# Kernel optimization log

Measured on AMD Instinct MI355X. Metric: run time of the kernel, lower is better.

Reference implementation:

```python
import jax, jax.numpy as jnp
import numpy as np

V, EMB, ENC, DEC = 50000, 256, 512, 512
E2 = ENC * 2            # bidirectional encoder output dim = 1024
B, S1, S2 = 128, 200, 200
NEG = -1e10


def _bahdanau(hidden, enc_out, mask, W, b, v):
    # hidden [B,DEC], enc_out [S,B,E2], mask [B,S] -> weights [B,S]
    S = enc_out.shape[0]
    h = jnp.broadcast_to(hidden[None], (S,) + hidden.shape)          # [S,B,DEC]
    energy = jnp.tanh(jnp.concatenate([h, enc_out], axis=-1) @ W + b)  # [S,B,DEC]
    scores = energy @ v                                              # [S,B]
    scores = jnp.where(mask.T == 0, NEG, scores)
    return jax.nn.softmax(scores, axis=0).T                          # [B,S]


def setup_inputs() -> dict:
    key = jax.random.key(0)
    ks = jax.random.split(key, 20)
    f = lambda k, shp, s=0.05: jax.random.normal(k, shp, dtype=jnp.float32) * s
    inp = {
        "input": jax.random.randint(ks[0], (B,), 0, V),
        "hidden": f(ks[1], (B, DEC), 1.0),
        "src1": jax.random.randint(ks[2], (S1, B), 0, V),
        "encoder_outputs1": f(ks[3], (S1, B, E2), 1.0),
        "mask1": jnp.ones((B, S1), dtype=jnp.int32),
        "triple_mask": jnp.ones((B, S1), dtype=jnp.int32),
        "encoder_outputs2": f(ks[4], (S2, B, E2), 1.0),
        "mask2": jnp.ones((B, S2), dtype=jnp.int32),
        # parameters
        "embedding": f(ks[5], (V, EMB)),
        "attn_W": f(ks[6], (E2 + DEC, DEC)),
        "attn_b": jnp.zeros((DEC,), jnp.float32),
        "attn_v": f(ks[7], (DEC,)),
        "copy_W": f(ks[8], (E2 + DEC, DEC)),
        "copy_b": jnp.zeros((DEC,), jnp.float32),
        "copy_v": f(ks[9], (DEC,)),
        "gru_Wih": f(ks[10], (3 * DEC, E2 + EMB)),
        "gru_Whh": f(ks[11], (3 * DEC, DEC)),
        "gru_bih": jnp.zeros((3 * DEC,), jnp.float32),
        "gru_bhh": jnp.zeros((3 * DEC,), jnp.float32),
        "fc_W": f(ks[12], (V, E2 + DEC)),
        "fc_b": jnp.zeros((V,), jnp.float32),
        "gate_W": f(ks[13], (1, E2 + EMB)),
        "gate_b": jnp.zeros((1,), jnp.float32),
    }
    return inp


def reference(input, hidden, src1, encoder_outputs1, mask1, triple_mask,
              encoder_outputs2, mask2, embedding, attn_W, attn_b, attn_v,
              copy_W, copy_b, copy_v, gru_Wih, gru_Whh, gru_bih, gru_bhh,
              fc_W, fc_b, gate_W, gate_b):
    # embed current token (dropout = identity at eval)
    emb = embedding[input]                                           # [B,EMB]
    # joint attention over concatenated encoders
    enc = jnp.concatenate([encoder_outputs1, encoder_outputs2], axis=0)  # [S1+S2,B,E2]
    mask = jnp.concatenate([mask1, mask2], axis=1)                   # [B,S1+S2]
    a = _bahdanau(hidden, enc, mask, attn_W, attn_b, attn_v)         # [B,S1+S2]
    weighted = jnp.einsum('bs,sbe->be', a, enc)                      # [B,E2]
    # single-step GRU (PyTorch gate layout: r, z, n)
    x = jnp.concatenate([emb, weighted], axis=-1)                    # [B,E2+EMB]
    gx = x @ gru_Wih.T + gru_bih
    gh = hidden @ gru_Whh.T + gru_bhh
    xr, xz, xn = jnp.split(gx, 3, axis=-1)
    hr, hz, hn = jnp.split(gh, 3, axis=-1)
    r = jax.nn.sigmoid(xr + hr)
    z = jax.nn.sigmoid(xz + hz)
    n = jnp.tanh(xn + r * hn)
    h_new = (1.0 - z) * n + z * hidden                               # [B,DEC]
    # generation distribution
    state = jnp.concatenate([h_new, weighted], axis=1)               # [B,DEC+E2]
    vocab_dist = jax.nn.softmax(state @ fc_W.T + fc_b, axis=-1)      # [B,V]
    # copy gate + copy attention over encoder 1 only
    p_gen = jax.nn.sigmoid(jnp.concatenate([weighted, emb], axis=-1) @ gate_W.T + gate_b)  # [B,1]
    attn_dist = _bahdanau(h_new, encoder_outputs1, mask1 * triple_mask,
                          copy_W, copy_b, copy_v)                    # [B,S1]
    vd = p_gen * vocab_dist
    ad = (1.0 - p_gen) * attn_dist
    # scatter_add copy probabilities into vocab slots
    b_idx = jnp.arange(vd.shape[0])[:, None]                         # [B,1]
    final_dist = vd.at[b_idx, src1.T].add(ad)                        # [B,V]
    return final_dist, h_new
```

## Files before the change

kernel.cpp:

```cpp
#include <hip/hip_runtime.h>
#include <math.h>

#define BB   128
#define DECD 512
#define E2D  1024
#define EMBD 256
#define S1D  200
#define S2D  200
#define SJD  400
#define VV   50000
#define NEGV (-1e10f)
#define JY   800

typedef unsigned short u16;
typedef __bf16 bf16x8 __attribute__((ext_vector_type(8)));
typedef float f32x4 __attribute__((ext_vector_type(4)));
typedef u16 u16x8 __attribute__((ext_vector_type(8)));

__device__ __forceinline__ u16 f2bf(float x) {
  unsigned u = __float_as_uint(x);
  unsigned r = (u + 0x7fffu + ((u >> 16) & 1u)) >> 16;
  return (u16)r;
}
__device__ __forceinline__ float bf2f(u16 h) {
  return __uint_as_float(((unsigned)h) << 16);
}

typedef const __attribute__((address_space(1))) void* gas_t;
typedef __attribute__((address_space(3))) void* las_t;
__device__ __forceinline__ void async_copy16(const u16* g, u16* l) {
  __builtin_amdgcn_global_load_lds((gas_t)g, (las_t)l, 16, 0, 0);
}

__global__ __launch_bounds__(256) void k_cvt(const float* __restrict__ src,
    u16* __restrict__ dst, int n8) {
  int i = blockIdx.x * 256 + threadIdx.x;
  if (i >= n8) return;
  const float4 f0 = *(const float4*)(src + (size_t)i * 8);
  const float4 f1 = *(const float4*)(src + (size_t)i * 8 + 4);
  u16x8 o;
  o[0] = f2bf(f0.x); o[1] = f2bf(f0.y); o[2] = f2bf(f0.z); o[3] = f2bf(f0.w);
  o[4] = f2bf(f1.x); o[5] = f2bf(f1.y); o[6] = f2bf(f1.z); o[7] = f2bf(f1.w);
  *(u16x8*)(dst + (size_t)i * 8) = o;
}

__global__ __launch_bounds__(256) void k_wt2(const float* __restrict__ Wa,
    const float* __restrict__ Wc, u16* __restrict__ Wta, u16* __restrict__ Wtc) {
  __shared__ float t[32][33];
  const float* W = blockIdx.z ? Wc : Wa;
  u16* Wt = blockIdx.z ? Wtc : Wta;
  int bk = blockIdx.x, bn = blockIdx.y;
  int tx = threadIdx.x & 31, ty = threadIdx.x >> 5;
  #pragma unroll
  for (int r = 0; r < 4; ++r) {
    int k = bk * 32 + ty + r * 8;
    t[ty + r * 8][tx] = W[(size_t)(512 + k) * 512 + bn * 32 + tx];
  }
  __syncthreads();
  #pragma unroll
  for (int r = 0; r < 4; ++r) {
    int n = bn * 32 + ty + r * 8;
    Wt[(size_t)n * 1024 + bk * 32 + tx] = f2bf(t[tx][ty + r * 8]);
  }
}

__global__ __launch_bounds__(256) void gemm_energy_jc(
    const float* __restrict__ enc1, const float* __restrict__ enc2,
    const u16* __restrict__ BtA, const u16* __restrict__ BtC,
    const float* __restrict__ hW, const float* __restrict__ v,
    float* __restrict__ partJ, float* __restrict__ preC) {
  __shared__ u16 As[2][64 * 32];
  __shared__ u16 Bs[256 * 32];
  __shared__ float sbuf[64][2];
  int tid = threadIdx.x;
  int wid = tid >> 6, lane = tid & 63;
  int wr = wid >> 1, wc = wid & 1;
  int bn = blockIdx.x;
  int jy = blockIdx.y;
  int joint = (jy < JY);
  size_t m0 = joint ? (size_t)jy * 64 : (size_t)(jy - JY) * 64;
  int bhalf = (jy & 1) * 64;
  int n0 = bn * 256;

  int rA = tid >> 2, cslot = tid & 3;
  int lAoff = rA * 32 + ((cslot ^ ((rA >> 1) & 3)) * 8);
  const float* base;
  if (joint)
    base = (m0 < (size_t)S1D * BB) ? (enc1 + m0 * E2D)
                                   : (enc2 + (m0 - (size_t)S1D * BB) * E2D);
  else
    base = enc1 + m0 * E2D;
  const float* gA_f = base + (size_t)rA * E2D + cslot * 8;

  const u16* Bt = joint ? BtA : BtC;
  const u16* gB[4];
  #pragma unroll
  for (int i = 0; i < 4; ++i) {
    int rn = i * 64 + wid * 16 + (lane >> 2);
    int c = (lane & 3) ^ ((rn >> 1) & 3);
    gB[i] = Bt + (size_t)(n0 + rn) * E2D + c * 8;
  }

  int q = lane >> 4, cl = lane & 15;
  int aoff[2], boff[8];
  #pragma unroll
  for (int mi = 0; mi < 2; ++mi) {
    int row = wr * 32 + mi * 16 + cl;
    aoff[mi] = row * 64 + ((q ^ ((row >> 1) & 3)) * 16);
  }
  #pragma unroll
  for (int nj = 0; nj < 8; ++nj) {
    int rn = wc * 128 + nj * 16 + cl;
    boff[nj] = rn * 64 + ((q ^ ((rn >> 1) & 3)) * 16);
  }

  f32x4 acc[2][8];
  #pragma unroll
  for (int mi = 0; mi < 2; ++mi)
    #pragma unroll
    for (int nj = 0; nj < 8; ++nj) {
      f32x4 z = {0.f, 0.f, 0.f, 0.f};
      acc[mi][nj] = z;
    }

  float4 a0 = *(const float4*)(gA_f);
  float4 a1 = *(const float4*)(gA_f + 4);
  {
    u16x8 ob;
    ob[0] = f2bf(a0.x); ob[1] = f2bf(a0.y); ob[2] = f2bf(a0.z); ob[3] = f2bf(a0.w);
    ob[4] = f2bf(a1.x); ob[5] = f2bf(a1.y); ob[6] = f2bf(a1.z); ob[7] = f2bf(a1.w);
    *(u16x8*)(&As[0][lAoff]) = ob;
  }
  a0 = *(const float4*)(gA_f + 32);
  a1 = *(const float4*)(gA_f + 36);

  for (int t = 0; t < 32; ++t) {
    int cur = t & 1, nxt = cur ^ 1;
    int k0 = t * 32, k1 = k0 + 32;
    #pragma unroll
    for (int i = 0; i < 4; ++i) async_copy16(gB[i] + k0, &Bs[2048 * i + wid * 512]);
    if (t < 31) {
      u16x8 ob;
      ob[0] = f2bf(a0.x); ob[1] = f2bf(a0.y); ob[2] = f2bf(a0.z); ob[3] = f2bf(a0.w);
      ob[4] = f2bf(a1.x); ob[5] = f2bf(a1.y); ob[6] = f2bf(a1.z); ob[7] = f2bf(a1.w);
      *(u16x8*)(&As[nxt][lAoff]) = ob;
      if (t < 30) {
        a0 = *(const float4*)(gA_f + k1 + 32);
        a1 = *(const float4*)(gA_f + k1 + 36);
      }
    }
    __syncthreads();
    bf16x8 af[2];
    #pragma unroll
    for (int mi = 0; mi < 2; ++mi)
      af[mi] = *(const bf16x8*)((const char*)As[cur] + aoff[mi]);
    #pragma unroll
    for (int nj = 0; nj < 8; ++nj) {
      bf16x8 bg = *(const bf16x8*)((const char*)Bs + boff[nj]);
      acc[0][nj] = __builtin_amdgcn_mfma_f32_16x16x32_bf16(af[0], bg, acc[0][nj], 0, 0, 0);
      acc[1][nj] = __builtin_amdgcn_mfma_f32_16x16x32_bf16(af[1], bg, acc[1][nj], 0, 0, 0);
    }
    __syncthreads();
  }

  if (joint) {
    #pragma unroll
    for (int mi = 0; mi < 2; ++mi) {
      #pragma unroll
      for (int j = 0; j < 4; ++j) {
        int m = wr * 32 + mi * 16 + q * 4 + j;
        float s = 0.f;
        #pragma unroll
        for (int nj = 0; nj < 8; ++nj) {
          int d = n0 + wc * 128 + nj * 16 + cl;
          s += tanhf(acc[mi][nj][j] + hW[(size_t)(bhalf + m) * DECD + d]) * v[d];
        }
        s += __shfl_xor(s, 1, 64);
        s += __shfl_xor(s, 2, 64);
        s += __shfl_xor(s, 4, 64);
        s += __shfl_xor(s, 8, 64);
        if (cl == 0) sbuf[m][wc] = s;
      }
    }
    __syncthreads();
    if (tid < 64)
      partJ[(size_t)bn * 51200 + m0 + tid] = sbuf[tid][0] + sbuf[tid][1];
  } else {
    #pragma unroll
    for (int mi = 0; mi < 2; ++mi) {
      #pragma unroll
      for (int nj = 0; nj < 8; ++nj) {
        int d = n0 + wc * 128 + nj * 16 + cl;
        #pragma unroll
        for (int j = 0; j < 4; ++j) {
          int m = wr * 32 + mi * 16 + q * 4 + j;
          preC[(m0 + m) * (size_t)DECD + d] = acc[mi][nj][j];
        }
      }
    }
  }
}

__global__ __launch_bounds__(256) void k_copy_epi(const float* __restrict__ preC,
    const float* __restrict__ hWc, const float* __restrict__ v,
    float* __restrict__ scC) {
  int r = blockIdx.x * 4 + (threadIdx.x >> 6);
  int lane = threadIdx.x & 63;
  int b = r & 127, s = r >> 7;
  const float* pr = preC + (size_t)r * DECD + lane * 8;
  const float* hr = hWc + (size_t)b * DECD + lane * 8;
  const float* vr = v + lane * 8;
  float4 p0 = *(const float4*)(pr),     p1 = *(const float4*)(pr + 4);
  float4 h0 = *(const float4*)(hr),     h1 = *(const float4*)(hr + 4);
  float4 v0 = *(const float4*)(vr),     v1 = *(const float4*)(vr + 4);
  float acc = tanhf(p0.x + h0.x) * v0.x + tanhf(p0.y + h0.y) * v0.y
            + tanhf(p0.z + h0.z) * v0.z + tanhf(p0.w + h0.w) * v0.w
            + tanhf(p1.x + h1.x) * v1.x + tanhf(p1.y + h1.y) * v1.y
            + tanhf(p1.z + h1.z) * v1.z + tanhf(p1.w + h1.w) * v1.w;
  #pragma unroll
  for (int off = 32; off > 0; off >>= 1) acc += __shfl_xor(acc, off, 64);
  if (lane == 0) scC[(size_t)b * S1D + s] = acc;
}

__global__ __launch_bounds__(256) void k_softmax_j(const float* __restrict__ part,
    int M, float* __restrict__ sc,
    const int* __restrict__ m1, const int* __restrict__ m2) {
  int b = blockIdx.x, tid = threadIdx.x;
  __shared__ float sm[4];
  int s0 = tid, s2 = tid + 256;
  float a0 = -INFINITY, a1 = -INFINITY;
  {
    int msk = (s0 < S1D) ? m1[b * S1D + s0] : m2[b * S2D + (s0 - S1D)];
    int m = s0 * 128 + b;
    a0 = msk ? (part[m] + part[M + m]) : NEGV;
  }
  if (s2 < SJD) {
    int msk = (s2 < S1D) ? m1[b * S1D + s2] : m2[b * S2D + (s2 - S1D)];
    int m = s2 * 128 + b;
    a1 = msk ? (part[m] + part[M + m]) : NEGV;
  }
  float vmax = fmaxf(a0, a1);
  #pragma unroll
  for (int off = 32; off > 0; off >>= 1) vmax = fmaxf(vmax, __shfl_down(vmax, off, 64));
  int lane = tid & 63, wid = tid >> 6;
  if (lane == 0) sm[wid] = vmax;
  __syncthreads();
  vmax = fmaxf(fmaxf(sm[0], sm[1]), fmaxf(sm[2], sm[3]));
  __syncthreads();
  float lsum = expf(a0 - vmax);
  if (s2 < SJD) lsum += expf(a1 - vmax);
  #pragma unroll
  for (int off = 32; off > 0; off >>= 1) lsum += __shfl_down(lsum, off, 64);
  if (lane == 0) sm[wid] = lsum;
  __syncthreads();
  float inv = 1.0f / (sm[0] + sm[1] + sm[2] + sm[3]);
  sc[(size_t)b * SJD + s0] = expf(a0 - vmax) * inv;
  if (s2 < SJD) sc[(size_t)b * SJD + s2] = expf(a1 - vmax) * inv;
}

__global__ __launch_bounds__(256) void k_softmax_s(float* __restrict__ sc, int S,
    const int* __restrict__ m1, const int* __restrict__ m2) {
  int b = blockIdx.x, tid = threadIdx.x;
  __shared__ float sm[4];
  int s0 = tid;
  float a0 = -INFINITY;
  if (s0 < S) {
    int msk = m1[b * S + s0] * m2[b * S + s0];
    a0 = msk ? sc[(size_t)b * S + s0] : NEGV;
  }
  float vmax = a0;
  #pragma unroll
  for (int off = 32; off > 0; off >>= 1) vmax = fmaxf(vmax, __shfl_down(vmax, off, 64));
  int lane = tid & 63, wid = tid >> 6;
  if (lane == 0) sm[wid] = vmax;
  __syncthreads();
  vmax = fmaxf(fmaxf(sm[0], sm[1]), fmaxf(sm[2], sm[3]));
  __syncthreads();
  float lsum = (s0 < S) ? expf(a0 - vmax) : 0.f;
  #pragma unroll
  for (int off = 32; off > 0; off >>= 1) lsum += __shfl_down(lsum, off, 64);
  if (lane == 0) sm[wid] = lsum;
  __syncthreads();
  float inv = 1.0f / (sm[0] + sm[1] + sm[2] + sm[3]);
  if (s0 < S) sc[(size_t)b * S + s0] = expf(a0 - vmax) * inv;
}

__device__ __forceinline__ void fc2_body(
    const u16* __restrict__ A, const float* __restrict__ Bf,
    const float* __restrict__ bias, float* __restrict__ C,
    int N, int K, int n0) {
  __shared__ u16 As[2][128 * 32];
  __shared__ u16 Bs[2][128 * 32];
  int tid = threadIdx.x;
  int wid = tid >> 6, lane = tid & 63;
  int wr = wid >> 2, wc = wid & 3;

  int rowa = wid * 16 + (lane >> 2);
  int ca = (lane & 3) ^ ((rowa >> 1) & 3);
  const u16* gA = A + (size_t)rowa * K + ca * 8;

  int rB = tid >> 2, cB = tid & 3;
  int gnB = n0 + rB; if (gnB >= N) gnB = N - 1;
  const float* gB = Bf + (size_t)gnB * K + cB * 8;
  int lBoff = rB * 32 + ((cB ^ ((rB >> 1) & 3)) * 8);

  int q = lane >> 4, cl = lane & 15;
  int aoff[4], boff[2];
  #pragma unroll
  for (int mi = 0; mi < 4; ++mi) {
    int row = wr * 64 + mi * 16 + cl;
    aoff[mi] = row * 64 + ((q ^ ((row >> 1) & 3)) * 16);
  }
  #pragma unroll
  for (int nj = 0; nj < 2; ++nj) {
    int rn = wc * 32 + nj * 16 + cl;
    boff[nj] = rn * 64 + ((q ^ ((rn >> 1) & 3)) * 16);
  }

  f32x4 acc[4][2];
  #pragma unroll
  for (int mi = 0; mi < 4; ++mi)
    #pragma unroll
    for (int nj = 0; nj < 2; ++nj) {
      f32x4 z = {0.f, 0.f, 0.f, 0.f};
      acc[mi][nj] = z;
    }

  for (int k0 = 0; k0 < K; k0 += 64) {
    float4 b00 = *(const float4*)(gB + k0);
    float4 b01 = *(const float4*)(gB + k0 + 4);
    float4 b10 = *(const float4*)(gB + k0 + 32);
    float4 b11 = *(const float4*)(gB + k0 + 36);
    u16x8 o0, o1;
    o0[0] = f2bf(b00.x); o0[1] = f2bf(b00.y); o0[2] = f2bf(b00.z); o0[3] = f2bf(b00.w);
    o0[4] = f2bf(b01.x); o0[5] = f2bf(b01.y); o0[6] = f2bf(b01.z); o0[7] = f2bf(b01.w);
    o1[0] = f2bf(b10.x); o1[1] = f2bf(b10.y); o1[2] = f2bf(b10.z); o1[3] = f2bf(b10.w);
    o1[4] = f2bf(b11.x); o1[5] = f2bf(b11.y); o1[6] = f2bf(b11.z); o1[7] = f2bf(b11.w);
    *(u16x8*)(&Bs[0][lBoff]) = o0;
    *(u16x8*)(&Bs[1][lBoff]) = o1;
    async_copy16(gA + k0,      &As[0][wid * 512]);
    async_copy16(gA + k0 + 32, &As[1][wid * 512]);
    __syncthreads();
    #pragma unroll
    for (int h = 0; h < 2; ++h) {
      bf16x8 af[4], bg[2];
      #pragma unroll
      for (int mi = 0; mi < 4; ++mi) af[mi] = *(const bf16x8*)((const char*)As[h] + aoff[mi]);
      #pragma unroll
      for (int nj = 0; nj < 2; ++nj) bg[nj] = *(const bf16x8*)((const char*)Bs[h] + boff[nj]);
      #pragma unroll
      for (int mi = 0; mi < 4; ++mi)
        #pragma unroll
        for (int nj = 0; nj < 2; ++nj)
          acc[mi][nj] = __builtin_amdgcn_mfma_f32_16x16x32_bf16(af[mi], bg[nj], acc[mi][nj], 0, 0, 0);
    }
    __syncthreads();
  }

  #pragma unroll
  for (int mi = 0; mi < 4; ++mi) {
    #pragma unroll
    for (int nj = 0; nj < 2; ++nj) {
      int n = n0 + wc * 32 + nj * 16 + cl;
      if (n < N) {
        float bv = bias[n];
        #pragma unroll
        for (int j = 0; j < 4; ++j) {
          int m = wr * 64 + mi * 16 + q * 4 + j;
          C[(size_t)m * N + n] = acc[mi][nj][j] + bv;
        }
      }
    }
  }
}

__global__ __launch_bounds__(512) void gemm_gru(
    const u16* __restrict__ x_bf, const float* __restrict__ Wih,
    const float* __restrict__ bih, float* __restrict__ gx,
    const u16* __restrict__ h_bf, const float* __restrict__ Whh,
    const float* __restrict__ bhh, float* __restrict__ gh) {
  if (blockIdx.x < 12)
    fc2_body(x_bf, Wih, bih, gx, 1536, 1280, blockIdx.x * 128);
  else
    fc2_body(h_bf, Whh, bhh, gh, 1536, 512, (blockIdx.x - 12) * 128);
}

__global__ __launch_bounds__(512) void gemm_fc3(
    const u16* __restrict__ A, const float* __restrict__ Bf,
    const float* __restrict__ bias, float* __restrict__ C,
    int N, int K) {
  __shared__ u16 As[2][128 * 32];
  __shared__ u16 Bs[2][64 * 32];
  int tid = threadIdx.x;
  int wid = tid >> 6, lane = tid & 63;
  int wr = wid >> 2, wc = wid & 3;
  int n0 = blockIdx.x * 64;

  int rowa = wid * 16 + (lane >> 2);
  int ca = (lane & 3) ^ ((rowa >> 1) & 3);
  const u16* gA = A + (size_t)rowa * K + ca * 8;

  int rB = tid >> 3, cB = tid & 7;
  int gnB = n0 + rB; if (gnB >= N) gnB = N - 1;
  const float* gB = Bf + (size_t)gnB * K + cB * 8;
  int hB = cB >> 2, s4 = cB & 3;
  int lBoff = rB * 32 + ((s4 ^ ((rB >> 1) & 3)) * 8);

  int q = lane >> 4, cl = lane & 15;
  int aoff[4], boff;
  #pragma unroll
  for (int mi = 0; mi < 4; ++mi) {
    int row = wr * 64 + mi * 16 + cl;
    aoff[mi] = row * 64 + ((q ^ ((row >> 1) & 3)) * 16);
  }
  {
    int rn = wc * 16 + cl;
    boff = rn * 64 + ((q ^ ((rn >> 1) & 3)) * 16);
  }

  f32x4 acc[4];
  #pragma unroll
  for (int mi = 0; mi < 4; ++mi) {
    f32x4 z = {0.f, 0.f, 0.f, 0.f};
    acc[mi] = z;
  }

  for (int k0 = 0; k0 < K; k0 += 64) {
    float4 b0 = *(const float4*)(gB + k0);
    float4 b1 = *(const float4*)(gB + k0 + 4);
    u16x8 ob;
    ob[0] = f2bf(b0.x); ob[1] = f2bf(b0.y); ob[2] = f2bf(b0.z); ob[3] = f2bf(b0.w);
    ob[4] = f2bf(b1.x); ob[5] = f2bf(b1.y); ob[6] = f2bf(b1.z); ob[7] = f2bf(b1.w);
    *(u16x8*)(&Bs[hB][lBoff]) = ob;
    async_copy16(gA + k0,      &As[0][wid * 512]);
    async_copy16(gA + k0 + 32, &As[1][wid * 512]);
    __syncthreads();
    #pragma unroll
    for (int h = 0; h < 2; ++h) {
      bf16x8 af[4];
      #pragma unroll
      for (int mi = 0; mi < 4; ++mi) af[mi] = *(const bf16x8*)((const char*)As[h] + aoff[mi]);
      bf16x8 bg = *(const bf16x8*)((const char*)Bs[h] + boff);
      #pragma unroll
      for (int mi = 0; mi < 4; ++mi)
        acc[mi] = __builtin_amdgcn_mfma_f32_16x16x32_bf16(af[mi], bg, acc[mi], 0, 0, 0);
    }
    __syncthreads();
  }

  int n = n0 + wc * 16 + cl;
  if (n < N) {
    float bv = bias[n];
    #pragma unroll
    for (int mi = 0; mi < 4; ++mi)
      #pragma unroll
      for (int j = 0; j < 4; ++j) {
        int m = wr * 64 + mi * 16 + q * 4 + j;
        C[(size_t)m * N + n] = acc[mi][j] + bv;
      }
  }
}

__global__ __launch_bounds__(256) void k_partial(const float* __restrict__ h,
    const float* __restrict__ W, const float* __restrict__ bias,
    float* __restrict__ out) {
  int b = blockIdx.y;
  int d = blockIdx.x * 256 + threadIdx.x;
  const float* hr = h + (size_t)b * DECD;
  float acc = bias[d];
  #pragma unroll 8
  for (int k = 0; k < DECD; ++k) acc += hr[k] * W[(size_t)k * DECD + d];
  out[(size_t)b * DECD + d] = acc;
}

__global__ __launch_bounds__(256) void k_wpart(const float* __restrict__ enc1,
    const float* __restrict__ enc2, const float* __restrict__ a,
    float* __restrict__ wp) {
  int b = blockIdx.x;
  int e2 = blockIdx.y * 256 + threadIdx.x;
  int scn = blockIdx.z;
  const float* arow = a + (size_t)b * SJD;
  float acc0 = 0.f, acc1 = 0.f;
  #pragma unroll 4
  for (int s = scn * 100; s < scn * 100 + 100; ++s) {
    const float* ep = (s < S1D) ? (enc1 + ((size_t)s * BB + b) * E2D)
                                : (enc2 + ((size_t)(s - S1D) * BB + b) * E2D);
    float2 u = *(const float2*)(ep + e2 * 2);
    float w = arow[s];
    acc0 += w * u.x;
    acc1 += w * u.y;
  }
  float* dst = wp + ((size_t)scn * BB + b) * E2D + e2 * 2;
  dst[0] = acc0;
  dst[1] = acc1;
}

__global__ __launch_bounds__(256) void k_wsum_x(const float* __restrict__ wp,
    float* __restrict__ wgt, u16* __restrict__ x) {
  int i = blockIdx.x * 256 + threadIdx.x;
  const int NN = BB * E2D;
  float s = wp[i] + wp[NN + i] + wp[2 * NN + i] + wp[3 * NN + i];
  wgt[i] = s;
  int b = i >> 10, e = i & 1023;
  x[(size_t)b * 1280 + EMBD + e] = f2bf(s);
}

__global__ __launch_bounds__(256) void k_embx(const int* __restrict__ inp,
    const float* __restrict__ table, u16* __restrict__ x) {
  int b = blockIdx.x, t = threadIdx.x;
  x[(size_t)b * 1280 + t] = f2bf(table[(size_t)inp[b] * EMBD + t]);
}

__global__ __launch_bounds__(256) void k_gru_concat(const float* __restrict__ gx,
    const float* __restrict__ gh, const float* __restrict__ hidden,
    const float* __restrict__ wgt, float* __restrict__ hnew,
    u16* __restrict__ st) {
  int b = blockIdx.x, tid = threadIdx.x;
  #pragma unroll
  for (int qq = 0; qq < 2; ++qq) {
    int d = tid + qq * 256;
    size_t o = (size_t)b * 1536;
    float xr = gx[o + d],        hr = gh[o + d];
    float xz = gx[o + 512 + d],  hz = gh[o + 512 + d];
    float xn = gx[o + 1024 + d], hn = gh[o + 1024 + d];
    float r = 1.f / (1.f + expf(-(xr + hr)));
    float z = 1.f / (1.f + expf(-(xz + hz)));
    float n = tanhf(xn + r * hn);
    float hv = (1.f - z) * n + z * hidden[(size_t)b * DECD + d];
    hnew[(size_t)b * DECD + d] = hv;
    st[(size_t)b * 1536 + d] = f2bf(hv);
  }
  #pragma unroll
  for (int qq = 0; qq < 4; ++qq) {
    int e = tid + qq * 256;
    st[(size_t)b * 1536 + DECD + e] = f2bf(wgt[(size_t)b * E2D + e]);
  }
}

__global__ __launch_bounds__(256) void k_pgen(const float* __restrict__ wgt,
    const int* __restrict__ inp, const float* __restrict__ table,
    const float* __restrict__ gW, const float* __restrict__ gb,
    float* __restrict__ pg) {
  int b = blockIdx.x, tid = threadIdx.x;
  __shared__ float sm[4];
  float s = 0.f;
  for (int k = tid; k < E2D + EMBD; k += 256)
    s += gW[k] * ((k < E2D) ? wgt[(size_t)b * E2D + k]
                            : table[(size_t)inp[b] * EMBD + k - E2D]);
  #pragma unroll
  for (int off = 32; off > 0; off >>= 1) s += __shfl_down(s, off, 64);
  int lane = tid & 63, wid = tid >> 6;
  if (lane == 0) sm[wid] = s;
  __syncthreads();
  if (tid == 0) {
    float t = sm[0] + sm[1] + sm[2] + sm[3] + gb[0];
    pg[b] = 1.f / (1.f + expf(-t));
  }
}

__global__ __launch_bounds__(256) void k_vocab_sc(float* __restrict__ dist,
    const float* __restrict__ pg, const float* __restrict__ ad,
    const int* __restrict__ src1) {
  int b = blockIdx.x, tid = threadIdx.x;
  float* row = dist + (size_t)b * VV;
  __shared__ float sm[4];
  float m = -INFINITY;
  for (int i = tid; i < VV; i += 256) m = fmaxf(m, row[i]);
  #pragma unroll
  for (int off = 32; off > 0; off >>= 1) m = fmaxf(m, __shfl_down(m, off, 64));
  int lane = tid & 63, wid = tid >> 6;
  if (lane == 0) sm[wid] = m;
  __syncthreads();
  m = fmaxf(fmaxf(sm[0], sm[1]), fmaxf(sm[2], sm[3]));
  __syncthreads();
  float s = 0.f;
  for (int i = tid; i < VV; i += 256) s += expf(row[i] - m);
  #pragma unroll
  for (int off = 32; off > 0; off >>= 1) s += __shfl_down(s, off, 64);
  if (lane == 0) sm[wid] = s;
  __syncthreads();
  s = sm[0] + sm[1] + sm[2] + sm[3];
  float pgb = pg[b];
  float scale = pgb / s;
  for (int i = tid; i < VV; i += 256) row[i] = expf(row[i] - m) * scale;
  __syncthreads();
  if (tid < S1D) {
    float val = (1.f - pgb) * ad[(size_t)b * S1D + tid];
    int tok = src1[(size_t)tid * BB + b];
    atomicAdd(&row[tok], val);
  }
}

extern "C" void kernel_launch(void* const* d_in, const int* in_sizes, int n_in,
                              void* d_out, int out_size, void* d_ws, size_t ws_size,
                              hipStream_t stream) {
  (void)in_sizes; (void)n_in; (void)out_size; (void)ws_size;
  const int*   input  = (const int*)d_in[0];
  const float* hidden = (const float*)d_in[1];
  const int*   src1   = (const int*)d_in[2];
  const float* enc1   = (const float*)d_in[3];
  const int*   mask1  = (const int*)d_in[4];
  const int*   triple = (const int*)d_in[5];
  const float* enc2   = (const float*)d_in[6];
  const int*   mask2  = (const int*)d_in[7];
  const float* embedding = (const float*)d_in[8];
  const float* attn_W = (const float*)d_in[9];
  const float* attn_b = (const float*)d_in[10];
  const float* attn_v = (const float*)d_in[11];
  const float* copy_W = (const float*)d_in[12];
  const float* copy_b = (const float*)d_in[13];
  const float* copy_v = (const float*)d_in[14];
  const float* gru_Wih = (const float*)d_in[15];
  const float* gru_Whh = (const float*)d_in[16];
  const float* gru_bih = (const float*)d_in[17];
  const float* gru_bhh = (const float*)d_in[18];
  const float* fc_W   = (const float*)d_in[19];
  const float* fc_b   = (const float*)d_in[20];
  const float* gate_W = (const float*)d_in[21];
  const float* gate_b = (const float*)d_in[22];

  char* w = (char*)d_ws;
  u16* Wt_a = (u16*)w;                w += (size_t)512 * 1024 * 2;
  u16* Wt_c = (u16*)w;                w += (size_t)512 * 1024 * 2;
  float* partJ = (float*)w;           w += (size_t)2 * 51200 * 4;
  float* preC = (float*)w;            w += (size_t)25600 * 512 * 4;
  float* hWa  = (float*)w;            w += (size_t)BB * DECD * 4;
  float* hWc  = (float*)w;            w += (size_t)BB * DECD * 4;
  float* scJ  = (float*)w;            w += (size_t)BB * SJD * 4;
  float* scC  = (float*)w;            w += (size_t)BB * S1D * 4;
  float* wgt  = (float*)w;            w += (size_t)BB * E2D * 4;
  float* wpart = (float*)w;           w += (size_t)4 * BB * E2D * 4;
  u16*   x_bf = (u16*)w;              w += (size_t)BB * 1280 * 2;
  u16*   hid_bf = (u16*)w;            w += (size_t)BB * DECD * 2;
  float* gx   = (float*)w;            w += (size_t)BB * 1536 * 4;
  float* gh   = (float*)w;            w += (size_t)BB * 1536 * 4;
  u16*   st_bf = (u16*)w;             w += (size_t)BB * 1536 * 2;
  float* pg   = (float*)w;            w += 512;

  float* out  = (float*)d_out;
  float* hnew = out + (size_t)BB * VV;

  k_wt2<<<dim3(32, 16, 2), 256, 0, stream>>>(attn_W, copy_W, Wt_a, Wt_c);
  k_cvt<<<32, 256, 0, stream>>>(hidden, hid_bf, BB * DECD / 8);
  k_partial<<<dim3(2, BB), 256, 0, stream>>>(hidden, attn_W, attn_b, hWa);
  k_embx<<<BB, 256, 0, stream>>>(input, embedding, x_bf);

  gemm_energy_jc<<<dim3(2, JY + 400), 256, 0, stream>>>(
      enc1, enc2, Wt_a, Wt_c, hWa, attn_v, partJ, preC);
  k_softmax_j<<<BB, 256, 0, stream>>>(partJ, 51200, scJ, mask1, mask2);

  k_wpart<<<dim3(BB, 2, 4), 256, 0, stream>>>(enc1, enc2, scJ, wpart);
  k_wsum_x<<<512, 256, 0, stream>>>(wpart, wgt, x_bf);

  gemm_gru<<<24, 512, 0, stream>>>(x_bf, gru_Wih, gru_bih, gx,
                                   hid_bf, gru_Whh, gru_bhh, gh);
  k_gru_concat<<<BB, 256, 0, stream>>>(gx, gh, hidden, wgt, hnew, st_bf);

  gemm_fc3<<<(VV + 63) / 64, 512, 0, stream>>>(st_bf, fc_W, fc_b, out, VV, 1536);

  k_pgen<<<BB, 256, 0, stream>>>(wgt, input, embedding, gate_W, gate_b, pg);
  k_partial<<<dim3(2, BB), 256, 0, stream>>>(hnew, copy_W, copy_b, hWc);
  k_copy_epi<<<25600 / 4, 256, 0, stream>>>(preC, hWc, copy_v, scC);
  k_softmax_s<<<BB, 256, 0, stream>>>(scC, S1D, mask1, triple);

  k_vocab_sc<<<BB, 256, 0, stream>>>(out, pg, scC, src1);
}
```

Before: 598.6 us.

## Fuse prep kernels and merge softmaxes into consumer kernels to cut launches

Merges the weight transpose, hidden conversion, attention partial GEMV and embedding gather into one launch. The joint softmax moves into the weighted-sum kernel, which recomputes it redundantly per block, and the copy softmax moves into the vocab scatter kernel. The p_gen and copy partial kernels are combined into one launch. Also adds a register prefetch of B in one GEMM and uses native bf16 conversion. This saves several launches and scJ round trips but repeats the softmax reduction across 8 blocks per batch row.

```diff
diff --git a/kernel.cpp b/kernel.cpp
--- a/kernel.cpp
+++ b/kernel.cpp
@@ -25,6 +25,12 @@
 __device__ __forceinline__ float bf2f(u16 h) {
   return __uint_as_float(((unsigned)h) << 16);
 }
+__device__ __forceinline__ u16x8 cvt8h(float4 a, float4 b) {
+  bf16x8 r;
+  r[0] = (__bf16)a.x; r[1] = (__bf16)a.y; r[2] = (__bf16)a.z; r[3] = (__bf16)a.w;
+  r[4] = (__bf16)b.x; r[5] = (__bf16)b.y; r[6] = (__bf16)b.z; r[7] = (__bf16)b.w;
+  return *reinterpret_cast<u16x8*>(&r);
+}
 
 typedef const __attribute__((address_space(1))) void* gas_t;
 typedef __attribute__((address_space(3))) void* las_t;
@@ -32,35 +38,49 @@
   __builtin_amdgcn_global_load_lds((gas_t)g, (las_t)l, 16, 0, 0);
 }
 
-__global__ __launch_bounds__(256) void k_cvt(const float* __restrict__ src,
-    u16* __restrict__ dst, int n8) {
-  int i = blockIdx.x * 256 + threadIdx.x;
-  if (i >= n8) return;
-  const float4 f0 = *(const float4*)(src + (size_t)i * 8);
-  const float4 f1 = *(const float4*)(src + (size_t)i * 8 + 4);
-  u16x8 o;
-  o[0] = f2bf(f0.x); o[1] = f2bf(f0.y); o[2] = f2bf(f0.z); o[3] = f2bf(f0.w);
-  o[4] = f2bf(f1.x); o[5] = f2bf(f1.y); o[6] = f2bf(f1.z); o[7] = f2bf(f1.w);
-  *(u16x8*)(dst + (size_t)i * 8) = o;
-}
-
-__global__ __launch_bounds__(256) void k_wt2(const float* __restrict__ Wa,
-    const float* __restrict__ Wc, u16* __restrict__ Wta, u16* __restrict__ Wtc) {
-  __shared__ float t[32][33];
-  const float* W = blockIdx.z ? Wc : Wa;
-  u16* Wt = blockIdx.z ? Wtc : Wta;
-  int bk = blockIdx.x, bn = blockIdx.y;
-  int tx = threadIdx.x & 31, ty = threadIdx.x >> 5;
-  #pragma unroll
-  for (int r = 0; r < 4; ++r) {
-    int k = bk * 32 + ty + r * 8;
-    t[ty + r * 8][tx] = W[(size_t)(512 + k) * 512 + bn * 32 + tx];
-  }
-  __syncthreads();
-  #pragma unroll
-  for (int r = 0; r < 4; ++r) {
-    int n = bn * 32 + ty + r * 8;
-    Wt[(size_t)n * 1024 + bk * 32 + tx] = f2bf(t[tx][ty + r * 8]);
+__global__ __launch_bounds__(256) void k_prep(
+    const float* __restrict__ Wa, const float* __restrict__ Wc,
+    u16* __restrict__ Wta, u16* __restrict__ Wtc,
+    const float* __restrict__ hidden, u16* __restrict__ hid_bf,
+    const float* __restrict__ attn_b, float* __restrict__ hWa,
+    const int* __restrict__ inp, const float* __restrict__ table,
+    u16* __restrict__ x_bf) {
+  int blk = blockIdx.x, tid = threadIdx.x;
+  if (blk < 1024) {
+    __shared__ float t[32][33];
+    int z = blk >> 9, rem = blk & 511;
+    int bk = rem & 31, bn = rem >> 5;
+    const float* W = z ? Wc : Wa;
+    u16* Wt = z ? Wtc : Wta;
+    int tx = tid & 31, ty = tid >> 5;
+    #pragma unroll
+    for (int r = 0; r < 4; ++r) {
+      int k = bk * 32 + ty + r * 8;
+      t[ty + r * 8][tx] = W[(size_t)(512 + k) * 512 + bn * 32 + tx];
+    }
+    __syncthreads();
+    #pragma unroll
+    for (int r = 0; r < 4; ++r) {
+      int n = bn * 32 + ty + r * 8;
+      Wt[(size_t)n * 1024 + bk * 32 + tx] = f2bf(t[tx][ty + r * 8]);
+    }
+  } else if (blk < 1056) {
+    int i = (blk - 1024) * 256 + tid;
+    const float4 f0 = *(const float4*)(hidden + (size_t)i * 8);
+    const float4 f1 = *(const float4*)(hidden + (size_t)i * 8 + 4);
+    *(u16x8*)(hid_bf + (size_t)i * 8) = cvt8h(f0, f1);
+  } else if (blk < 1312) {
+    int idx = blk - 1056;
+    int b = idx >> 1;
+    int d = (idx & 1) * 256 + tid;
+    const float* hr = hidden + (size_t)b * DECD;
+    float acc = attn_b[d];
+    #pragma unroll 8
+    for (int k = 0; k < DECD; ++k) acc += hr[k] * Wa[(size_t)k * DECD + d];
+    hWa[(size_t)b * DECD + d] = acc;
+  } else {
+    int b = blk - 1312;
+    x_bf[(size_t)b * 1280 + tid] = f2bf(table[(size_t)inp[b] * EMBD + tid]);
   }
 }
 
@@ -125,12 +145,7 @@
 
   float4 a0 = *(const float4*)(gA_f);
   float4 a1 = *(const float4*)(gA_f + 4);
-  {
-    u16x8 ob;
-    ob[0] = f2bf(a0.x); ob[1] = f2bf(a0.y); ob[2] = f2bf(a0.z); ob[3] = f2bf(a0.w);
-    ob[4] = f2bf(a1.x); ob[5] = f2bf(a1.y); ob[6] = f2bf(a1.z); ob[7] = f2bf(a1.w);
-    *(u16x8*)(&As[0][lAoff]) = ob;
-  }
+  *(u16x8*)(&As[0][lAoff]) = cvt8h(a0, a1);
   a0 = *(const float4*)(gA_f + 32);
   a1 = *(const float4*)(gA_f + 36);
 
@@ -140,10 +155,7 @@
     #pragma unroll
     for (int i = 0; i < 4; ++i) async_copy16(gB[i] + k0, &Bs[2048 * i + wid * 512]);
     if (t < 31) {
-      u16x8 ob;
-      ob[0] = f2bf(a0.x); ob[1] = f2bf(a0.y); ob[2] = f2bf(a0.z); ob[3] = f2bf(a0.w);
-      ob[4] = f2bf(a1.x); ob[5] = f2bf(a1.y); ob[6] = f2bf(a1.z); ob[7] = f2bf(a1.w);
-      *(u16x8*)(&As[nxt][lAoff]) = ob;
+      *(u16x8*)(&As[nxt][lAoff]) = cvt8h(a0, a1);
       if (t < 30) {
         a0 = *(const float4*)(gA_f + k1 + 32);
         a1 = *(const float4*)(gA_f + k1 + 36);
@@ -222,22 +234,26 @@
   if (lane == 0) scC[(size_t)b * S1D + s] = acc;
 }
 
-__global__ __launch_bounds__(256) void k_softmax_j(const float* __restrict__ part,
-    int M, float* __restrict__ sc,
-    const int* __restrict__ m1, const int* __restrict__ m2) {
+__global__ __launch_bounds__(256) void k_wpart_sm(const float* __restrict__ part,
+    const float* __restrict__ enc1, const float* __restrict__ enc2,
+    const int* __restrict__ m1, const int* __restrict__ m2,
+    float* __restrict__ wp) {
   int b = blockIdx.x, tid = threadIdx.x;
+  int e2 = blockIdx.y * 256 + tid;
+  int scn = blockIdx.z;
   __shared__ float sm[4];
+  __shared__ float ws[100];
   int s0 = tid, s2 = tid + 256;
-  float a0 = -INFINITY, a1 = -INFINITY;
+  float a0, a1 = -INFINITY;
   {
     int msk = (s0 < S1D) ? m1[b * S1D + s0] : m2[b * S2D + (s0 - S1D)];
     int m = s0 * 128 + b;
-    a0 = msk ? (part[m] + part[M + m]) : NEGV;
+    a0 = msk ? (part[m] + part[51200 + m]) : NEGV;
   }
   if (s2 < SJD) {
     int msk = (s2 < S1D) ? m1[b * S1D + s2] : m2[b * S2D + (s2 - S1D)];
     int m = s2 * 128 + b;
-    a1 = msk ? (part[m] + part[M + m]) : NEGV;
+    a1 = msk ? (part[m] + part[51200 + m]) : NEGV;
   }
   float vmax = fmaxf(a0, a1);
   #pragma unroll
@@ -254,35 +270,38 @@
   if (lane == 0) sm[wid] = lsum;
   __syncthreads();
   float inv = 1.0f / (sm[0] + sm[1] + sm[2] + sm[3]);
-  sc[(size_t)b * SJD + s0] = expf(a0 - vmax) * inv;
-  if (s2 < SJD) sc[(size_t)b * SJD + s2] = expf(a1 - vmax) * inv;
-}
-
-__global__ __launch_bounds__(256) void k_softmax_s(float* __restrict__ sc, int S,
-    const int* __restrict__ m1, const int* __restrict__ m2) {
-  int b = blockIdx.x, tid = threadIdx.x;
-  __shared__ float sm[4];
-  int s0 = tid;
-  float a0 = -INFINITY;
-  if (s0 < S) {
-    int msk = m1[b * S + s0] * m2[b * S + s0];
-    a0 = msk ? sc[(size_t)b * S + s0] : NEGV;
-  }
-  float vmax = a0;
-  #pragma unroll
-  for (int off = 32; off > 0; off >>= 1) vmax = fmaxf(vmax, __shfl_down(vmax, off, 64));
-  int lane = tid & 63, wid = tid >> 6;
-  if (lane == 0) sm[wid] = vmax;
-  __syncthreads();
-  vmax = fmaxf(fmaxf(sm[0], sm[1]), fmaxf(sm[2], sm[3]));
-  __syncthreads();
-  float lsum = (s0 < S) ? expf(a0 - vmax) : 0.f;
-  #pragma unroll
-  for (int off = 32; off > 0; off >>= 1) lsum += __shfl_down(lsum, off, 64);
-  if (lane == 0) sm[wid] = lsum;
-  __syncthreads();
-  float inv = 1.0f / (sm[0] + sm[1] + sm[2] + sm[3]);
-  if (s0 < S) sc[(size_t)b * S + s0] = expf(a0 - vmax) * inv;
+  if (tid < 100) {
+    int s = scn * 100 + tid;
+    int msk = (s < S1D) ? m1[b * S1D + s] : m2[b * S2D + (s - S1D)];
+    int m = s * 128 + b;
+    float av = msk ? (part[m] + part[51200 + m]) : NEGV;
+    ws[tid] = expf(av - vmax) * inv;
+  }
+  __syncthreads();
+  float acc0 = 0.f, acc1 = 0.f;
+  #pragma unroll 4
+  for (int i = 0; i < 100; ++i) {
+    int s = scn * 100 + i;
+    const float* ep = (s < S1D) ? (enc1 + ((size_t)s * BB + b) * E2D)
+                                : (enc2 + ((size_t)(s - S1D) * BB + b) * E2D);
+    float2 u = *(const float2*)(ep + e2 * 2);
+    float w = ws[i];
+    acc0 += w * u.x;
+    acc1 += w * u.y;
+  }
+  float* dst = wp + ((size_t)scn * BB + b) * E2D + e2 * 2;
+  dst[0] = acc0;
+  dst[1] = acc1;
+}
+
+__global__ __launch_bounds__(256) void k_wsum_x(const float* __restrict__ wp,
+    float* __restrict__ wgt, u16* __restrict__ x) {
+  int i = blockIdx.x * 256 + threadIdx.x;
+  const int NN = BB * E2D;
+  float s = wp[i] + wp[NN + i] + wp[2 * NN + i] + wp[3 * NN + i];
+  wgt[i] = s;
+  int b = i >> 10, e = i & 1023;
+  x[(size_t)b * 1280 + EMBD + e] = f2bf(s);
 }
 
 __device__ __forceinline__ void fc2_body(
@@ -331,13 +350,8 @@
     float4 b01 = *(const float4*)(gB + k0 + 4);
     float4 b10 = *(const float4*)(gB + k0 + 32);
     float4 b11 = *(const float4*)(gB + k0 + 36);
-    u16x8 o0, o1;
-    o0[0] = f2bf(b00.x); o0[1] = f2bf(b00.y); o0[2] = f2bf(b00.z); o0[3] = f2bf(b00.w);
-    o0[4] = f2bf(b01.x); o0[5] = f2bf(b01.y); o0[6] = f2bf(b01.z); o0[7] = f2bf(b01.w);
-    o1[0] = f2bf(b10.x); o1[1] = f2bf(b10.y); o1[2] = f2bf(b10.z); o1[3] = f2bf(b10.w);
-    o1[4] = f2bf(b11.x); o1[5] = f2bf(b11.y); o1[6] = f2bf(b11.z); o1[7] = f2bf(b11.w);
-    *(u16x8*)(&Bs[0][lBoff]) = o0;
-    *(u16x8*)(&Bs[1][lBoff]) = o1;
+    *(u16x8*)(&Bs[0][lBoff]) = cvt8h(b00, b01);
+    *(u16x8*)(&Bs[1][lBoff]) = cvt8h(b10, b11);
     async_copy16(gA + k0,      &As[0][wid * 512]);
     async_copy16(gA + k0 + 32, &As[1][wid * 512]);
     __syncthreads();
@@ -425,16 +439,18 @@
     acc[mi] = z;
   }
 
+  float4 b0 = *(const float4*)(gB);
+  float4 b1 = *(const float4*)(gB + 4);
+
   for (int k0 = 0; k0 < K; k0 += 64) {
-    float4 b0 = *(const float4*)(gB + k0);
-    float4 b1 = *(const float4*)(gB + k0 + 4);
-    u16x8 ob;
-    ob[0] = f2bf(b0.x); ob[1] = f2bf(b0.y); ob[2] = f2bf(b0.z); ob[3] = f2bf(b0.w);
-    ob[4] = f2bf(b1.x); ob[5] = f2bf(b1.y); ob[6] = f2bf(b1.z); ob[7] = f2bf(b1.w);
-    *(u16x8*)(&Bs[hB][lBoff]) = ob;
+    *(u16x8*)(&Bs[hB][lBoff]) = cvt8h(b0, b1);
     async_copy16(gA + k0,      &As[0][wid * 512]);
     async_copy16(gA + k0 + 32, &As[1][wid * 512]);
     __syncthreads();
+    if (k0 + 64 < K) {
+      b0 = *(const float4*)(gB + k0 + 64);
+      b1 = *(const float4*)(gB + k0 + 68);
+    }
     #pragma unroll
     for (int h = 0; h < 2; ++h) {
       bf16x8 af[4];
@@ -459,56 +475,6 @@
         C[(size_t)m * N + n] = acc[mi][j] + bv;
       }
   }
-}
-
-__global__ __launch_bounds__(256) void k_partial(const float* __restrict__ h,
-    const float* __restrict__ W, const float* __restrict__ bias,
-    float* __restrict__ out) {
-  int b = blockIdx.y;
-  int d = blockIdx.x * 256 + threadIdx.x;
-  const float* hr = h + (size_t)b * DECD;
-  float acc = bias[d];
-  #pragma unroll 8
-  for (int k = 0; k < DECD; ++k) acc += hr[k] * W[(size_t)k * DECD + d];
-  out[(size_t)b * DECD + d] = acc;
-}
-
-__global__ __launch_bounds__(256) void k_wpart(const float* __restrict__ enc1,
-    const float* __restrict__ enc2, const float* __restrict__ a,
-    float* __restrict__ wp) {
-  int b = blockIdx.x;
-  int e2 = blockIdx.y * 256 + threadIdx.x;
-  int scn = blockIdx.z;
-  const float* arow = a + (size_t)b * SJD;
-  float acc0 = 0.f, acc1 = 0.f;
-  #pragma unroll 4
-  for (int s = scn * 100; s < scn * 100 + 100; ++s) {
-    const float* ep = (s < S1D) ? (enc1 + ((size_t)s * BB + b) * E2D)
-                                : (enc2 + ((size_t)(s - S1D) * BB + b) * E2D);
-    float2 u = *(const float2*)(ep + e2 * 2);
-    float w = arow[s];
-    acc0 += w * u.x;
-    acc1 += w * u.y;
-  }
-  float* dst = wp + ((size_t)scn * BB + b) * E2D + e2 * 2;
-  dst[0] = acc0;
-  dst[1] = acc1;
-}
-
-__global__ __launch_bounds__(256) void k_wsum_x(const float* __restrict__ wp,
-    float* __restrict__ wgt, u16* __restrict__ x) {
-  int i = blockIdx.x * 256 + threadIdx.x;
-  const int NN = BB * E2D;
-  float s = wp[i] + wp[NN + i] + wp[2 * NN + i] + wp[3 * NN + i];
-  wgt[i] = s;
-  int b = i >> 10, e = i & 1023;
-  x[(size_t)b * 1280 + EMBD + e] = f2bf(s);
-}
-
-__global__ __launch_bounds__(256) void k_embx(const int* __restrict__ inp,
-    const float* __restrict__ table, u16* __restrict__ x) {
-  int b = blockIdx.x, t = threadIdx.x;
-  x[(size_t)b * 1280 + t] = f2bf(table[(size_t)inp[b] * EMBD + t]);
 }
 
 __global__ __launch_bounds__(256) void k_gru_concat(const float* __restrict__ gx,
@@ -537,38 +503,53 @@
   }
 }
 
-__global__ __launch_bounds__(256) void k_pgen(const float* __restrict__ wgt,
+__global__ __launch_bounds__(256) void k_pgen_partial(const float* __restrict__ wgt,
     const int* __restrict__ inp, const float* __restrict__ table,
     const float* __restrict__ gW, const float* __restrict__ gb,
-    float* __restrict__ pg) {
-  int b = blockIdx.x, tid = threadIdx.x;
-  __shared__ float sm[4];
-  float s = 0.f;
-  for (int k = tid; k < E2D + EMBD; k += 256)
-    s += gW[k] * ((k < E2D) ? wgt[(size_t)b * E2D + k]
-                            : table[(size_t)inp[b] * EMBD + k - E2D]);
-  #pragma unroll
-  for (int off = 32; off > 0; off >>= 1) s += __shfl_down(s, off, 64);
-  int lane = tid & 63, wid = tid >> 6;
-  if (lane == 0) sm[wid] = s;
-  __syncthreads();
-  if (tid == 0) {
-    float t = sm[0] + sm[1] + sm[2] + sm[3] + gb[0];
-    pg[b] = 1.f / (1.f + expf(-t));
-  }
-}
-
-__global__ __launch_bounds__(256) void k_vocab_sc(float* __restrict__ dist,
-    const float* __restrict__ pg, const float* __restrict__ ad,
+    float* __restrict__ pg,
+    const float* __restrict__ hnew, const float* __restrict__ copy_W,
+    const float* __restrict__ copy_b, float* __restrict__ hWc) {
+  int tid = threadIdx.x;
+  if (blockIdx.x < 128) {
+    int b = blockIdx.x;
+    __shared__ float sm[4];
+    float s = 0.f;
+    for (int k = tid; k < E2D + EMBD; k += 256)
+      s += gW[k] * ((k < E2D) ? wgt[(size_t)b * E2D + k]
+                              : table[(size_t)inp[b] * EMBD + k - E2D]);
+    #pragma unroll
+    for (int off = 32; off > 0; off >>= 1) s += __shfl_down(s, off, 64);
+    int lane = tid & 63, wid = tid >> 6;
+    if (lane == 0) sm[wid] = s;
+    __syncthreads();
+    if (tid == 0) {
+      float t = sm[0] + sm[1] + sm[2] + sm[3] + gb[0];
+      pg[b] = 1.f / (1.f + expf(-t));
+    }
+  } else {
+    int idx = blockIdx.x - 128;
+    int b = idx >> 1;
+    int d = (idx & 1) * 256 + tid;
+    const float* hr = hnew + (size_t)b * DECD;
+    float acc = copy_b[d];
+    #pragma unroll 8
+    for (int k = 0; k < DECD; ++k) acc += hr[k] * copy_W[(size_t)k * DECD + d];
+    hWc[(size_t)b * DECD + d] = acc;
+  }
+}
+
+__global__ __launch_bounds__(256) void k_vocab_sc2(float* __restrict__ dist,
+    const float* __restrict__ pg, const float* __restrict__ scC,
+    const int* __restrict__ m1, const int* __restrict__ tr,
     const int* __restrict__ src1) {
   int b = blockIdx.x, tid = threadIdx.x;
   float* row = dist + (size_t)b * VV;
   __shared__ float sm[4];
+  int lane = tid & 63, wid = tid >> 6;
   float m = -INFINITY;
   for (int i = tid; i < VV; i += 256) m = fmaxf(m, row[i]);
   #pragma unroll
   for (int off = 32; off > 0; off >>= 1) m = fmaxf(m, __shfl_down(m, off, 64));
-  int lane = tid & 63, wid = tid >> 6;
   if (lane == 0) sm[wid] = m;
   __syncthreads();
   m = fmaxf(fmaxf(sm[0], sm[1]), fmaxf(sm[2], sm[3]));
@@ -584,8 +565,26 @@
   float scale = pgb / s;
   for (int i = tid; i < VV; i += 256) row[i] = expf(row[i] - m) * scale;
   __syncthreads();
+  float c0 = -INFINITY;
   if (tid < S1D) {
-    float val = (1.f - pgb) * ad[(size_t)b * S1D + tid];
+    int msk = m1[b * S1D + tid] * tr[b * S1D + tid];
+    c0 = msk ? scC[(size_t)b * S1D + tid] : NEGV;
+  }
+  float cmax = c0;
+  #pragma unroll
+  for (int off = 32; off > 0; off >>= 1) cmax = fmaxf(cmax, __shfl_down(cmax, off, 64));
+  if (lane == 0) sm[wid] = cmax;
+  __syncthreads();
+  cmax = fmaxf(fmaxf(sm[0], sm[1]), fmaxf(sm[2], sm[3]));
+  __syncthreads();
+  float csum = (tid < S1D) ? expf(c0 - cmax) : 0.f;
+  #pragma unroll
+  for (int off = 32; off > 0; off >>= 1) csum += __shfl_down(csum, off, 64);
+  if (lane == 0) sm[wid] = csum;
+  __syncthreads();
+  float cinv = 1.0f / (sm[0] + sm[1] + sm[2] + sm[3]);
+  if (tid < S1D) {
+    float val = (1.f - pgb) * expf(c0 - cmax) * cinv;
     int tok = src1[(size_t)tid * BB + b];
     atomicAdd(&row[tok], val);
   }
@@ -626,7 +625,6 @@
   float* preC = (float*)w;            w += (size_t)25600 * 512 * 4;
   float* hWa  = (float*)w;            w += (size_t)BB * DECD * 4;
   float* hWc  = (float*)w;            w += (size_t)BB * DECD * 4;
-  float* scJ  = (float*)w;            w += (size_t)BB * SJD * 4;
   float* scC  = (float*)w;            w += (size_t)BB * S1D * 4;
   float* wgt  = (float*)w;            w += (size_t)BB * E2D * 4;
   float* wpart = (float*)w;           w += (size_t)4 * BB * E2D * 4;
@@ -640,16 +638,14 @@
   float* out  = (float*)d_out;
   float* hnew = out + (size_t)BB * VV;
 
-  k_wt2<<<dim3(32, 16, 2), 256, 0, stream>>>(attn_W, copy_W, Wt_a, Wt_c);
-  k_cvt<<<32, 256, 0, stream>>>(hidden, hid_bf, BB * DECD / 8);
-  k_partial<<<dim3(2, BB), 256, 0, stream>>>(hidden, attn_W, attn_b, hWa);
-  k_embx<<<BB, 256, 0, stream>>>(input, embedding, x_bf);
+  k_prep<<<1440, 256, 0, stream>>>(attn_W, copy_W, Wt_a, Wt_c,
+                                   hidden, hid_bf, attn_b, hWa,
+                                   input, embedding, x_bf);
 
   gemm_energy_jc<<<dim3(2, JY + 400), 256, 0, stream>>>(
       enc1, enc2, Wt_a, Wt_c, hWa, attn_v, partJ, preC);
-  k_softmax_j<<<BB, 256, 0, stream>>>(partJ, 51200, scJ, mask1, mask2);
-
-  k_wpart<<<dim3(BB, 2, 4), 256, 0, stream>>>(enc1, enc2, scJ, wpart);
+
+  k_wpart_sm<<<dim3(BB, 2, 4), 256, 0, stream>>>(partJ, enc1, enc2, mask1, mask2, wpart);
   k_wsum_x<<<512, 256, 0, stream>>>(wpart, wgt, x_bf);
 
   gemm_gru<<<24, 512, 0, stream>>>(x_bf, gru_Wih, gru_bih, gx,
@@ -658,10 +654,9 @@
 
   gemm_fc3<<<(VV + 63) / 64, 512, 0, stream>>>(st_bf, fc_W, fc_b, out, VV, 1536);
 
-  k_pgen<<<BB, 256, 0, stream>>>(wgt, input, embedding, gate_W, gate_b, pg);
-  k_partial<<<dim3(2, BB), 256, 0, stream>>>(hnew, copy_W, copy_b, hWc);
+  k_pgen_partial<<<384, 256, 0, stream>>>(wgt, input, embedding, gate_W, gate_b, pg,
+                                          hnew, copy_W, copy_b, hWc);
   k_copy_epi<<<25600 / 4, 256, 0, stream>>>(preC, hWc, copy_v, scC);
-  k_softmax_s<<<BB, 256, 0, stream>>>(scC, S1D, mask1, triple);
-
-  k_vocab_sc<<<BB, 256, 0, stream>>>(out, pg, scC, src1);
-}
+
+  k_vocab_sc2<<<BB, 256, 0, stream>>>(out, pg, scC, mask1, triple, src1);
+}
```

Result: faster. 576.6 us (-3.7%).
